# Kernel tuning notes

Measured on AMD Instinct MI355X. Metric: run time of the kernel, lower is better.

Reference implementation:

```python
import jax, jax.numpy as jnp
import numpy as np

NUM_HEADS = 2
HIDDEN_DIM = 128  # == node_dim
HEAD_DIM = 64     # node_dim // num_heads
NEG_SLOPE = 0.2
N_NODES = 25000
N_EDGES = 400000
NODE_DIM = 128
EDGE_DIM = 64


def setup_inputs() -> dict:
    key = jax.random.key(0)
    ks = jax.random.split(key, 16)
    s = 0.05
    return {
        "node_features": jax.random.normal(ks[0], (N_NODES, NODE_DIM), jnp.float32),
        "edge_features": jax.random.normal(ks[1], (N_EDGES, EDGE_DIM), jnp.float32),
        "edge_index": jax.random.randint(ks[2], (2, N_EDGES), 0, N_NODES, jnp.int32),
        "ni_W": jax.random.normal(ks[3], (NODE_DIM, NUM_HEADS * HIDDEN_DIM), jnp.float32) * s,
        "ni_b": jax.random.normal(ks[4], (NUM_HEADS * HIDDEN_DIM,), jnp.float32) * s,
        "nj_W": jax.random.normal(ks[5], (NODE_DIM, NUM_HEADS * HIDDEN_DIM), jnp.float32) * s,
        "nj_b": jax.random.normal(ks[6], (NUM_HEADS * HIDDEN_DIM,), jnp.float32) * s,
        "e_W": jax.random.normal(ks[7], (EDGE_DIM, NUM_HEADS * HIDDEN_DIM), jnp.float32) * s,
        "e_b": jax.random.normal(ks[8], (NUM_HEADS * HIDDEN_DIM,), jnp.float32) * s,
        "attn_proj": jax.random.normal(ks[9], (NUM_HEADS, HIDDEN_DIM), jnp.float32),
        "msg_W": jax.random.normal(ks[10], (NODE_DIM + EDGE_DIM, NODE_DIM), jnp.float32) * s,
        "msg_b": jax.random.normal(ks[11], (NODE_DIM,), jnp.float32) * s,
        "out_W": jax.random.normal(ks[12], (NODE_DIM, NODE_DIM), jnp.float32) * s,
        "out_b": jax.random.normal(ks[13], (NODE_DIM,), jnp.float32) * s,
    }


def _scatter_softmax(logits, seg, num_segments):
    # logits: [E, H], seg: [E] -> per-destination-node softmax over incident edges
    seg_max = jax.ops.segment_max(logits, seg, num_segments=num_segments)  # [N, H]
    ex = jnp.exp(logits - seg_max[seg])
    denom = jax.ops.segment_sum(ex, seg, num_segments=num_segments)  # [N, H]
    return ex / denom[seg]


def reference(node_features, edge_features, edge_index, ni_W, ni_b, nj_W, nj_b,
              e_W, e_b, attn_proj, msg_W, msg_b, out_W, out_b):
    n_nodes = node_features.shape[0]
    dst = edge_index[0]  # aggregation index (indices()[0])
    src = edge_index[1]
    ni = node_features[dst]  # [E, D]
    nj = node_features[src]  # [E, D]

    hidden = ni @ ni_W + ni_b + nj @ nj_W + nj_b + edge_features @ e_W + e_b  # [E, H*hid]
    hidden = jnp.where(hidden >= 0, hidden, NEG_SLOPE * hidden)  # LeakyReLU
    hidden = hidden.reshape(-1, NUM_HEADS, HIDDEN_DIM)

    attn_logits = jnp.einsum('ehd,hd->eh', hidden, attn_proj)  # [E, H]
    attn = _scatter_softmax(attn_logits, dst, n_nodes)  # [E, H]

    messages = jnp.concatenate((nj, edge_features), axis=-1) @ msg_W + msg_b  # [E, D]
    messages = messages.reshape(-1, NUM_HEADS, HEAD_DIM) * attn[:, :, None]
    agg = jax.ops.segment_sum(messages, dst, num_segments=n_nodes)  # [N, H, head]
    agg = agg.reshape(n_nodes, NUM_HEADS * HEAD_DIM)
    return agg @ out_W + out_b
```

## Files before the change

kernel.cpp:

```cpp
#include <hip/hip_runtime.h>

#define NEG 0.2f
typedef unsigned short u16;
typedef __bf16 bf8 __attribute__((ext_vector_type(8)));
typedef float f4 __attribute__((ext_vector_type(4)));
typedef u16 u16x8 __attribute__((ext_vector_type(8)));

#define OFF_P16   0ull
#define SZ_P16    (25000ull*256ull)
#define OFF_PM16  (OFF_P16 + SZ_P16)
#define SZ_PM16   (25000ull*64ull)
#define OFF_BCF   (OFF_PM16 + SZ_PM16)
#define SZ_BCF    40960ull
#define OFF_BTOT  (OFF_BCF + SZ_BCF)
#define SZ_BTOT   256ull
#define OFF_EX    (OFF_BTOT + SZ_BTOT)
#define SZ_EX     (2ull*400000ull)
#define OFF_DEN   (OFF_EX + SZ_EX)
#define SZ_DEN    (2ull*25000ull)
#define OFF_AGG   (OFF_DEN + SZ_DEN)
#define SZ_AGG    (25000ull*128ull)
#define OFF_CNT   (OFF_AGG + SZ_AGG)
#define SZ_CNT    25000ull
#define OFF_CUR   (OFF_CNT + SZ_CNT)
#define SZ_CUR    25000ull
#define OFF_PERM  (OFF_CUR + SZ_CUR)
#define SZ_PERM   400000ull
#define OFF_DST   (OFF_PERM + SZ_PERM)
#define SZ_DST    400000ull
#define OFF_SRC   (OFF_DST + SZ_DST)
#define SZ_SRC    400000ull
#define OFF_EWF   (OFF_SRC + SZ_SRC)
#define SZ_EWF    8192ull
#define OFF_MWF   (OFF_EWF + SZ_EWF)
#define SZ_MWF    4096ull

__device__ __forceinline__ u16 f2b(float f) {
    unsigned u = __float_as_uint(f);
    return (u16)((u + 0x7FFFu + ((u >> 16) & 1u)) >> 16);
}
__device__ __forceinline__ float b2f(u16 v) {
    return __uint_as_float(((unsigned)v) << 16);
}
__device__ __forceinline__ bf8 pack8(float4 a, float4 b) {
    union { u16 u[8]; bf8 v; } x;
    x.u[0] = f2b(a.x); x.u[1] = f2b(a.y); x.u[2] = f2b(a.z); x.u[3] = f2b(a.w);
    x.u[4] = f2b(b.x); x.u[5] = f2b(b.y); x.u[6] = f2b(b.z); x.u[7] = f2b(b.w);
    return x.v;
}

__global__ void k_prep(const float* __restrict__ niW, const float* __restrict__ njW,
                       const float* __restrict__ msgW, const float* __restrict__ eW,
                       const float* __restrict__ nib, const float* __restrict__ njb,
                       const float* __restrict__ eb,
                       u16* __restrict__ bcf, float* __restrict__ btot,
                       u16* __restrict__ ewfrag, u16* __restrict__ msgfrag) {
    int idx = blockIdx.x * 256 + threadIdx.x;
    if (idx < 81920) {
        int fi = idx >> 9;
        int ln = (idx >> 3) & 63, i = idx & 7;
        int cb = fi >> 2, s = fi & 3;
        int k = s * 32 + ((ln >> 4) << 3) + i;
        int col = cb * 16 + (ln & 15);
        float v = (col < 256) ? niW[k * 256 + col]
                : (col < 512) ? njW[k * 256 + (col - 256)]
                              : msgW[k * 128 + (col - 512)];
        bcf[idx] = f2b(v);
    }
    if (idx < 16384) {
        int c = idx >> 10, s = (idx >> 9) & 1, ln = (idx >> 3) & 63, i = idx & 7;
        int k = s * 32 + ((ln >> 4) << 3) + i;
        int col = c * 16 + (ln & 15);
        ewfrag[idx] = f2b(eW[k * 256 + col]);
    }
    if (idx < 8192) {
        int c = idx >> 10, s = (idx >> 9) & 1, ln = (idx >> 3) & 63, i = idx & 7;
        int k = s * 32 + ((ln >> 4) << 3) + i;
        int col = c * 16 + (ln & 15);
        msgfrag[idx] = f2b(msgW[(128 + k) * 128 + col]);
    }
    if (idx < 256) btot[idx] = nib[idx] + njb[idx] + eb[idx];
}

__device__ __forceinline__ void gemm_tile(const float* Al, int astride, int acol0,
                                          const float* Bl, int trow, int tcol,
                                          float acc[4][8]) {
    for (int k4 = 0; k4 < 64; k4 += 4) {
        float ar[4][4];
#pragma unroll
        for (int r = 0; r < 4; ++r)
            *(float4*)ar[r] = *(const float4*)&Al[(trow * 4 + r) * astride + acol0 + k4];
#pragma unroll
        for (int kk = 0; kk < 4; ++kk) {
            float4 b0 = *(const float4*)&Bl[(k4 + kk) * 128 + tcol * 8];
            float4 b1 = *(const float4*)&Bl[(k4 + kk) * 128 + tcol * 8 + 4];
            float bv[8] = {b0.x, b0.y, b0.z, b0.w, b1.x, b1.y, b1.z, b1.w};
#pragma unroll
            for (int r = 0; r < 4; ++r) {
                float av = ar[r][kk];
#pragma unroll
                for (int j = 0; j < 8; ++j) acc[r][j] = fmaf(av, bv[j], acc[r][j]);
            }
        }
    }
}

__global__ __launch_bounds__(256) void k_node_pre(const float* __restrict__ nf,
                                                  const u16* __restrict__ bcf,
                                                  u16* __restrict__ pre16,
                                                  u16* __restrict__ premsg16) {
    int t = threadIdx.x, w = t >> 6, l = t & 63;
    int n0 = blockIdx.x * 64 + w * 16;
    int rsel = l & 15, kb = l >> 4;
    int nA = n0 + rsel;
    size_t nAc = (nA < 25000) ? (size_t)nA : 24999;
    const float* ap = &nf[nAc * 128 + kb * 8];
    bf8 a[4];
#pragma unroll
    for (int s = 0; s < 4; ++s) {
        float4 x = *(const float4*)&ap[s * 32];
        float4 y = *(const float4*)&ap[s * 32 + 4];
        a[s] = pack8(x, y);
    }
    int nC = n0 + kb * 4;
#pragma unroll 4
    for (int cb = 0; cb < 40; ++cb) {
        f4 acc = {0.f, 0.f, 0.f, 0.f};
#pragma unroll
        for (int s = 0; s < 4; ++s) {
            bf8 b = *(const bf8*)&bcf[(size_t)((cb * 4 + s) * 64 + l) * 8];
            acc = __builtin_amdgcn_mfma_f32_16x16x32_bf16(a[s], b, acc, 0, 0, 0);
        }
#pragma unroll
        for (int r = 0; r < 4; ++r) {
            int nn = nC + r;
            if (nn < 25000) {
                if (cb < 32) pre16[(size_t)nn * 512 + cb * 16 + rsel] = f2b(acc[r]);
                else premsg16[(size_t)nn * 128 + (cb - 32) * 16 + rsel] = f2b(acc[r]);
            }
        }
    }
}

__global__ void k_hist(const int* __restrict__ eidx, int* __restrict__ count) {
    int e = blockIdx.x * 256 + threadIdx.x;
    if (e < 400000) atomicAdd(&count[eidx[e]], 1);
}

__global__ __launch_bounds__(1024) void k_scan(const int* __restrict__ count,
                                               int* __restrict__ cursor) {
    __shared__ int sums[1024];
    int t = threadIdx.x;
    int base = t * 25;
    int v[25];
    int local = 0;
#pragma unroll
    for (int i = 0; i < 25; ++i) {
        int idx = base + i;
        int c = (idx < 25000) ? count[idx] : 0;
        v[i] = local;
        local += c;
    }
    sums[t] = local;
    __syncthreads();
    for (int off = 1; off < 1024; off <<= 1) {
        int x = (t >= off) ? sums[t - off] : 0;
        __syncthreads();
        sums[t] += x;
        __syncthreads();
    }
    int prefix = (t == 0) ? 0 : sums[t - 1];
#pragma unroll
    for (int i = 0; i < 25; ++i) {
        int idx = base + i;
        if (idx < 25000) cursor[idx] = prefix + v[i];
    }
}

__global__ void k_scatter(const int* __restrict__ eidx, int* __restrict__ cursor,
                          int* __restrict__ perm, int* __restrict__ dsts,
                          int* __restrict__ srcs) {
    int e = blockIdx.x * 256 + threadIdx.x;
    if (e < 400000) {
        int d = eidx[e];
        int p = atomicAdd(&cursor[d], 1);
        perm[p] = e;
        dsts[p] = d;
        srcs[p] = eidx[400000 + e];
    }
}

__global__ __launch_bounds__(256) void k_edge_logits(
        const float* __restrict__ ef, const int* __restrict__ perm,
        const int* __restrict__ dsts, const int* __restrict__ srcs,
        const u16* __restrict__ ewfrag, const u16* __restrict__ pre16,
        const float* __restrict__ btot, const float* __restrict__ aproj,
        float* __restrict__ exs, float* __restrict__ denom) {
    __shared__ int eperm[64], dstl[64], srcl[64];
    int t = threadIdx.x;
    int w = t >> 6, l = t & 63;
    int p0 = blockIdx.x * 64;
    int row = l & 15, kb = l >> 4;

    if (t < 64) {
        eperm[t] = perm[p0 + t];
        dstl[t] = dsts[p0 + t];
        srcl[t] = srcs[p0 + t];
    }
    __syncthreads();

    int ea = eperm[w * 16 + row];
    const float* ap = &ef[(size_t)ea * 64 + kb * 8];
    float4 a00 = *(const float4*)ap;
    float4 a01 = *(const float4*)(ap + 4);
    float4 a10 = *(const float4*)(ap + 32);
    float4 a11 = *(const float4*)(ap + 36);
    bf8 a0 = pack8(a00, a01), a1 = pack8(a10, a11);

    int ed[4], es[4];
#pragma unroll
    for (int r = 0; r < 4; ++r) {
        int i4 = w * 16 + kb * 4 + r;
        ed[r] = dstl[i4];
        es[r] = srcl[i4];
    }

    float part0[4] = {0.f, 0.f, 0.f, 0.f}, part1[4] = {0.f, 0.f, 0.f, 0.f};
#pragma unroll
    for (int c = 0; c < 16; ++c) {
        bf8 b0 = *(const bf8*)&ewfrag[(size_t)((c * 2 + 0) * 64 + l) * 8];
        bf8 b1 = *(const bf8*)&ewfrag[(size_t)((c * 2 + 1) * 64 + l) * 8];
        f4 acc = {0.f, 0.f, 0.f, 0.f};
        acc = __builtin_amdgcn_mfma_f32_16x16x32_bf16(a0, b0, acc, 0, 0, 0);
        acc = __builtin_amdgcn_mfma_f32_16x16x32_bf16(a1, b1, acc, 0, 0, 0);
        int col = c * 16 + row;
        float bt = btot[col], apj = aproj[col];
#pragma unroll
        for (int r = 0; r < 4; ++r) {
            float pi = b2f(pre16[(size_t)ed[r] * 512 + col]);
            float pj = b2f(pre16[(size_t)es[r] * 512 + 256 + col]);
            float hid = acc[r] + pi + pj + bt;
            hid = hid >= 0.f ? hid : NEG * hid;
            if (c < 8) part0[r] = fmaf(hid, apj, part0[r]);
            else       part1[r] = fmaf(hid, apj, part1[r]);
        }
    }
#pragma unroll
    for (int m = 1; m < 16; m <<= 1) {
#pragma unroll
        for (int r = 0; r < 4; ++r) {
            part0[r] += __shfl_xor(part0[r], m);
            part1[r] += __shfl_xor(part1[r], m);
        }
    }
    if (row == 0) {
#pragma unroll
        for (int r = 0; r < 4; ++r) {
            int p = p0 + w * 16 + kb * 4 + r;
            float e0 = __expf(part0[r]);
            float e1 = __expf(part1[r]);
            exs[(size_t)p * 2 + 0] = e0;
            exs[(size_t)p * 2 + 1] = e1;
            atomicAdd(&denom[ed[r] * 2 + 0], e0);
            atomicAdd(&denom[ed[r] * 2 + 1], e1);
        }
    }
}

__global__ __launch_bounds__(256) void k_messages(
        const float* __restrict__ ef, const int* __restrict__ perm,
        const int* __restrict__ dsts, const int* __restrict__ srcs,
        const u16* __restrict__ msgfrag, const u16* __restrict__ premsg16,
        const float* __restrict__ exs, const float* __restrict__ denom,
        float* __restrict__ agg) {
    __shared__ float Msg[64 * 132];
    __shared__ int dstl[64], srcl[64], eperm[64];
    __shared__ float attl[64][2];
    int t = threadIdx.x;
    int w = t >> 6, l = t & 63;
    int p0 = blockIdx.x * 64;
    int row = l & 15, kb = l >> 4;

    if (t < 64) {
        int p = p0 + t;
        eperm[t] = perm[p];
        int d = dsts[p];
        dstl[t] = d;
        srcl[t] = srcs[p];
        attl[t][0] = exs[(size_t)p * 2 + 0] / denom[d * 2 + 0];
        attl[t][1] = exs[(size_t)p * 2 + 1] / denom[d * 2 + 1];
    }
    __syncthreads();

    int ea = eperm[w * 16 + row];
    const float* apr = &ef[(size_t)ea * 64 + kb * 8];
    float4 a00 = *(const float4*)apr;
    float4 a01 = *(const float4*)(apr + 4);
    float4 a10 = *(const float4*)(apr + 32);
    float4 a11 = *(const float4*)(apr + 36);
    bf8 a0 = pack8(a00, a01), a1 = pack8(a10, a11);

    int esr[4];
    float at0[4], at1[4];
#pragma unroll
    for (int r = 0; r < 4; ++r) {
        int i4 = w * 16 + kb * 4 + r;
        esr[r] = srcl[i4];
        at0[r] = attl[i4][0];
        at1[r] = attl[i4][1];
    }

#pragma unroll
    for (int c = 0; c < 8; ++c) {
        bf8 b0 = *(const bf8*)&msgfrag[(size_t)((c * 2 + 0) * 64 + l) * 8];
        bf8 b1 = *(const bf8*)&msgfrag[(size_t)((c * 2 + 1) * 64 + l) * 8];
        f4 acc = {0.f, 0.f, 0.f, 0.f};
        acc = __builtin_amdgcn_mfma_f32_16x16x32_bf16(a0, b0, acc, 0, 0, 0);
        acc = __builtin_amdgcn_mfma_f32_16x16x32_bf16(a1, b1, acc, 0, 0, 0);
        int col = c * 16 + row;
#pragma unroll
        for (int r = 0; r < 4; ++r) {
            float m = acc[r] + b2f(premsg16[(size_t)esr[r] * 128 + col]);
            float wm = ((c < 4) ? at0[r] : at1[r]) * m;
            Msg[(w * 16 + kb * 4 + r) * 132 + col] = wm;
        }
    }
    __syncthreads();

    int c = t & 127, half = t >> 7;
    int r0 = half * 32, r1 = r0 + 32;
    int cur = dstl[r0];
    float sum = 0.f;
    for (int r = r0; r < r1; ++r) {
        int d = dstl[r];
        if (d != cur) {
            atomicAdd(&agg[(size_t)cur * 128 + c], sum);
            sum = 0.f;
            cur = d;
        }
        sum += Msg[r * 132 + c];
    }
    atomicAdd(&agg[(size_t)cur * 128 + c], sum);
}

__global__ __launch_bounds__(256) void k_out(
        const float* __restrict__ agg, const int* __restrict__ count,
        const float* __restrict__ msgb, const float* __restrict__ outW,
        const float* __restrict__ outb, float* __restrict__ out) {
    __shared__ float Al[64 * 128];
    __shared__ float Bl[64 * 128];
    int t = threadIdx.x, n0 = blockIdx.x * 64;
    int trow = t >> 4, tcol = t & 15;
#pragma unroll
    for (int q = 0; q < 8; ++q) {
        int g = t + 256 * q;
        int i = g >> 5, k4 = (g & 31) * 4;
        int n = n0 + i;
        float4 v = make_float4(0.f, 0.f, 0.f, 0.f);
        if (n < 25000) {
            v = *(const float4*)&agg[(size_t)n * 128 + k4];
            if (count[n] > 0) {
                float4 mb = *(const float4*)&msgb[k4];
                v.x += mb.x; v.y += mb.y; v.z += mb.z; v.w += mb.w;
            }
        }
        *(float4*)&Al[i * 128 + k4] = v;
    }
    float acc[4][8] = {};
    for (int kh = 0; kh < 2; ++kh) {
        __syncthreads();
#pragma unroll
        for (int q = 0; q < 8; ++q) {
            int g = t + 256 * q;
            int k = g >> 5, c4 = (g & 31) * 4;
            *(float4*)&Bl[k * 128 + c4] = *(const float4*)&outW[(kh * 64 + k) * 128 + c4];
        }
        __syncthreads();
        gemm_tile(Al, 128, kh * 64, Bl, trow, tcol, acc);
    }
    float ob[8];
    *(float4*)ob = *(const float4*)&outb[tcol * 8];
    *(float4*)(ob + 4) = *(const float4*)&outb[tcol * 8 + 4];
#pragma unroll
    for (int r = 0; r < 4; ++r) {
        int n = n0 + trow * 4 + r;
        if (n < 25000) {
            *(float4*)&out[(size_t)n * 128 + tcol * 8] =
                make_float4(acc[r][0] + ob[0], acc[r][1] + ob[1], acc[r][2] + ob[2], acc[r][3] + ob[3]);
            *(float4*)&out[(size_t)n * 128 + tcol * 8 + 4] =
                make_float4(acc[r][4] + ob[4], acc[r][5] + ob[5], acc[r][6] + ob[6], acc[r][7] + ob[7]);
        }
    }
}

extern "C" void kernel_launch(void* const* d_in, const int* in_sizes, int n_in,
                              void* d_out, int out_size, void* d_ws, size_t ws_size,
                              hipStream_t stream) {
    const float* nf    = (const float*)d_in[0];
    const float* ef    = (const float*)d_in[1];
    const int*   eidx  = (const int*)d_in[2];
    const float* niW   = (const float*)d_in[3];
    const float* nib   = (const float*)d_in[4];
    const float* njW   = (const float*)d_in[5];
    const float* njb   = (const float*)d_in[6];
    const float* eW    = (const float*)d_in[7];
    const float* eb    = (const float*)d_in[8];
    const float* aproj = (const float*)d_in[9];
    const float* msgW  = (const float*)d_in[10];
    const float* msgb  = (const float*)d_in[11];
    const float* outW  = (const float*)d_in[12];
    const float* outb  = (const float*)d_in[13];

    float* ws = (float*)d_ws;
    u16*   pre16     = (u16*)(ws + OFF_P16);
    u16*   premsg16  = (u16*)(ws + OFF_PM16);
    u16*   bcf       = (u16*)(ws + OFF_BCF);
    float* btot      = ws + OFF_BTOT;
    float* exs       = ws + OFF_EX;
    float* denom     = ws + OFF_DEN;
    float* agg       = ws + OFF_AGG;
    int*   count     = (int*)(ws + OFF_CNT);
    int*   cursor    = (int*)(ws + OFF_CUR);
    int*   perm      = (int*)(ws + OFF_PERM);
    int*   dsts      = (int*)(ws + OFF_DST);
    int*   srcs      = (int*)(ws + OFF_SRC);
    u16*   ewfrag    = (u16*)(ws + OFF_EWF);
    u16*   msgfrag   = (u16*)(ws + OFF_MWF);

    hipMemsetAsync(ws + OFF_DEN, 0, (size_t)(SZ_DEN + SZ_AGG + SZ_CNT) * 4, stream);

    k_prep<<<320, 256, 0, stream>>>(niW, njW, msgW, eW, nib, njb, eb,
                                    bcf, btot, ewfrag, msgfrag);
    k_node_pre<<<391, 256, 0, stream>>>(nf, bcf, pre16, premsg16);
    k_hist<<<1563, 256, 0, stream>>>(eidx, count);
    k_scan<<<1, 1024, 0, stream>>>(count, cursor);
    k_scatter<<<1563, 256, 0, stream>>>(eidx, cursor, perm, dsts, srcs);
    k_edge_logits<<<6250, 256, 0, stream>>>(ef, perm, dsts, srcs, ewfrag, pre16,
                                            btot, aproj, exs, denom);
    k_messages<<<6250, 256, 0, stream>>>(ef, perm, dsts, srcs, msgfrag, premsg16,
                                         exs, denom, agg);
    k_out<<<391, 256, 0, stream>>>(agg, count, msgb, outW, outb, (float*)d_out);
}
```

Baseline: 319.8 us.

## Transpose MFMA operands in edge-logit kernel so each lane owns one edge

Swaps the MFMA operand order so the output tile is laid out with edges along lanes and hidden columns along the accumulator registers. Each lane can then load its node's precomputed bf16 projections as contiguous 64-bit chunks, issued up front before the MFMA loop, instead of doing 128 scattered 16-bit gathers. The cross-lane reduction drops from a 4-step shuffle to 2 steps, and bias and attention vectors are read as vec4. It raises register pressure by holding 32 prefetched 64-bit values, and it relies on the weight fragment layout being correct in the swapped operand role.

Result: slower. 348.3 us (+8.9%).

```diff
diff --git a/kernel.cpp b/kernel.cpp
--- a/kernel.cpp
+++ b/kernel.cpp
@@ -200,7 +200,7 @@
     int t = threadIdx.x;
     int w = t >> 6, l = t & 63;
     int p0 = blockIdx.x * 64;
-    int row = l & 15, kb = l >> 4;
+    int le = l & 15, g4 = (l >> 4) << 2;
 
     if (t < 64) {
         eperm[t] = perm[p0 + t];
@@ -209,61 +209,63 @@
     }
     __syncthreads();
 
-    int ea = eperm[w * 16 + row];
-    const float* ap = &ef[(size_t)ea * 64 + kb * 8];
-    float4 a00 = *(const float4*)ap;
-    float4 a01 = *(const float4*)(ap + 4);
-    float4 a10 = *(const float4*)(ap + 32);
-    float4 a11 = *(const float4*)(ap + 36);
-    bf8 a0 = pack8(a00, a01), a1 = pack8(a10, a11);
-
-    int ed[4], es[4];
-#pragma unroll
-    for (int r = 0; r < 4; ++r) {
-        int i4 = w * 16 + kb * 4 + r;
-        ed[r] = dstl[i4];
-        es[r] = srcl[i4];
-    }
-
-    float part0[4] = {0.f, 0.f, 0.f, 0.f}, part1[4] = {0.f, 0.f, 0.f, 0.f};
+    int ie = w * 16 + le;
+    int ea = eperm[ie];
+    int ed = dstl[ie], es = srcl[ie];
+
+    const float* bp = &ef[(size_t)ea * 64 + (l >> 4) * 8];
+    float4 b00 = *(const float4*)bp;
+    float4 b01 = *(const float4*)(bp + 4);
+    float4 b10 = *(const float4*)(bp + 32);
+    float4 b11 = *(const float4*)(bp + 36);
+
+    const u16* pni = &pre16[(size_t)ed * 512 + g4];
+    const u16* pnj = &pre16[(size_t)es * 512 + 256 + g4];
+    unsigned long long pi[16], pj[16];
 #pragma unroll
     for (int c = 0; c < 16; ++c) {
-        bf8 b0 = *(const bf8*)&ewfrag[(size_t)((c * 2 + 0) * 64 + l) * 8];
-        bf8 b1 = *(const bf8*)&ewfrag[(size_t)((c * 2 + 1) * 64 + l) * 8];
+        pi[c] = *(const unsigned long long*)&pni[c * 16];
+        pj[c] = *(const unsigned long long*)&pnj[c * 16];
+    }
+
+    bf8 bf0 = pack8(b00, b01), bf1 = pack8(b10, b11);
+
+#pragma unroll
+    for (int c = 0; c < 16; ++c)
+        asm volatile("" :: "v"(pi[c]), "v"(pj[c]));
+    __builtin_amdgcn_sched_barrier(0);
+
+    float part0 = 0.f, part1 = 0.f;
+#pragma unroll
+    for (int c = 0; c < 16; ++c) {
+        bf8 wa0 = *(const bf8*)&ewfrag[(size_t)((c * 2 + 0) * 64 + l) * 8];
+        bf8 wa1 = *(const bf8*)&ewfrag[(size_t)((c * 2 + 1) * 64 + l) * 8];
         f4 acc = {0.f, 0.f, 0.f, 0.f};
-        acc = __builtin_amdgcn_mfma_f32_16x16x32_bf16(a0, b0, acc, 0, 0, 0);
-        acc = __builtin_amdgcn_mfma_f32_16x16x32_bf16(a1, b1, acc, 0, 0, 0);
-        int col = c * 16 + row;
-        float bt = btot[col], apj = aproj[col];
+        acc = __builtin_amdgcn_mfma_f32_16x16x32_bf16(wa0, bf0, acc, 0, 0, 0);
+        acc = __builtin_amdgcn_mfma_f32_16x16x32_bf16(wa1, bf1, acc, 0, 0, 0);
+        int colb = c * 16 + g4;
+        f4 bt4 = *(const f4*)&btot[colb];
+        f4 ap4 = *(const f4*)&aproj[colb];
+        float p = 0.f;
 #pragma unroll
         for (int r = 0; r < 4; ++r) {
-            float pi = b2f(pre16[(size_t)ed[r] * 512 + col]);
-            float pj = b2f(pre16[(size_t)es[r] * 512 + 256 + col]);
-            float hid = acc[r] + pi + pj + bt;
+            float hid = acc[r] + b2f((u16)(pi[c] >> (16 * r)))
+                               + b2f((u16)(pj[c] >> (16 * r))) + bt4[r];
             hid = hid >= 0.f ? hid : NEG * hid;
-            if (c < 8) part0[r] = fmaf(hid, apj, part0[r]);
-            else       part1[r] = fmaf(hid, apj, part1[r]);
-        }
-    }
-#pragma unroll
-    for (int m = 1; m < 16; m <<= 1) {
-#pragma unroll
-        for (int r = 0; r < 4; ++r) {
-            part0[r] += __shfl_xor(part0[r], m);
-            part1[r] += __shfl_xor(part1[r], m);
-        }
-    }
-    if (row == 0) {
-#pragma unroll
-        for (int r = 0; r < 4; ++r) {
-            int p = p0 + w * 16 + kb * 4 + r;
-            float e0 = __expf(part0[r]);
-            float e1 = __expf(part1[r]);
-            exs[(size_t)p * 2 + 0] = e0;
-            exs[(size_t)p * 2 + 1] = e1;
-            atomicAdd(&denom[ed[r] * 2 + 0], e0);
-            atomicAdd(&denom[ed[r] * 2 + 1], e1);
-        }
+            p = fmaf(hid, ap4[r], p);
+        }
+        if (c < 8) part0 += p; else part1 += p;
+    }
+    part0 += __shfl_xor(part0, 16); part0 += __shfl_xor(part0, 32);
+    part1 += __shfl_xor(part1, 16); part1 += __shfl_xor(part1, 32);
+    if (l < 16) {
+        int p = p0 + w * 16 + l;
+        float e0 = __expf(part0);
+        float e1 = __expf(part1);
+        exs[(size_t)p * 2 + 0] = e0;
+        exs[(size_t)p * 2 + 1] = e1;
+        atomicAdd(&denom[ed * 2 + 0], e0);
+        atomicAdd(&denom[ed * 2 + 1], e1);
     }
 }
 
```
